# Kernel optimization log

Hardware: AMD Instinct MI355X
Metric: run time of the kernel (lower is better)

## Reference

```python
import jax, jax.numpy as jnp
import numpy as np


def _binarize_ste(w):
    # forward: sign(w) in {-1, +1}; backward: identity (straight-through)
    wb = jnp.where(w >= 0, 1.0, -1.0).astype(w.dtype)
    return w + jax.lax.stop_gradient(wb - w)


def setup_inputs() -> dict:
    key = jax.random.key(0)
    k1, k2 = jax.random.split(key)
    IN, OUT, N = 2048, 2048, 8192
    x = jax.random.normal(k1, (N, IN), dtype=jnp.float32)
    # kaiming_uniform-like init: U(-bound, bound), bound = sqrt(6/in)*? (gain sqrt(5) default in torch)
    bound = float(np.sqrt(6.0 / IN))
    weight = jax.random.uniform(k2, (OUT, IN), dtype=jnp.float32, minval=-bound, maxval=bound)
    bias = jnp.zeros((OUT,), dtype=jnp.float32)
    return {"x": x, "weight": weight, "bias": bias}


def reference(x, weight, bias):
    w_binary = _binarize_ste(weight)  # [out, in], values in {-1, +1}
    # F.linear: x @ W^T + b
    return jnp.einsum('ni,oi->no', x, w_binary) + bias
```

## Files before the change

kernel.cpp:

```cpp
#include <hip/hip_runtime.h>
#include <stdint.h>


typedef __bf16 bf16x8 __attribute__((ext_vector_type(8)));
typedef float f32x16 __attribute__((ext_vector_type(16)));

typedef const __attribute__((address_space(1))) void* gas_ptr;
typedef __attribute__((address_space(3))) void* lds_ptr;

__device__ __forceinline__ unsigned short f2bf_rne(float f) {
    unsigned int u = __builtin_bit_cast(unsigned int, f);
    u += 0x7fffu + ((u >> 16) & 1u);
    return (unsigned short)(u >> 16);
}

__global__ __launch_bounds__(256) void cvt_x_kernel(const float* __restrict__ in,
                                                    unsigned short* __restrict__ out,
                                                    int n8) {
    int i = blockIdx.x * 256 + threadIdx.x;
    if (i >= n8) return;
    const float4* p = reinterpret_cast<const float4*>(in + (size_t)i * 8);
    float4 f0 = p[0], f1 = p[1];
    union { unsigned short s[8]; uint4 v; } o;
    o.s[0] = f2bf_rne(f0.x); o.s[1] = f2bf_rne(f0.y);
    o.s[2] = f2bf_rne(f0.z); o.s[3] = f2bf_rne(f0.w);
    o.s[4] = f2bf_rne(f1.x); o.s[5] = f2bf_rne(f1.y);
    o.s[6] = f2bf_rne(f1.z); o.s[7] = f2bf_rne(f1.w);
    *reinterpret_cast<uint4*>(out + (size_t)i * 8) = o.v;
}

__global__ __launch_bounds__(256) void bin_w_kernel(const float* __restrict__ in,
                                                    unsigned short* __restrict__ out,
                                                    int n4) {
    int i = blockIdx.x * 256 + threadIdx.x;
    if (i >= n4) return;
    float4 f = reinterpret_cast<const float4*>(in)[i];
    union { unsigned short s[4]; uint2 v; } o;
    o.s[0] = (f.x >= 0.f) ? 0x3F80u : 0xBF80u;
    o.s[1] = (f.y >= 0.f) ? 0x3F80u : 0xBF80u;
    o.s[2] = (f.z >= 0.f) ? 0x3F80u : 0xBF80u;
    o.s[3] = (f.w >= 0.f) ? 0x3F80u : 0xBF80u;
    reinterpret_cast<uint2*>(out)[i] = o.v;
}

#define TILE 128
#define BK   64

__global__ __launch_bounds__(256) void gemm_bin_kernel(
    const unsigned short* __restrict__ A,
    const unsigned short* __restrict__ B,
    const float* __restrict__ bias,
    float* __restrict__ C,
    int M, int N, int K)
{
    __shared__ __align__(16) unsigned char smem[32768];
    unsigned short* Als = (unsigned short*)smem;
    unsigned short* Bls = (unsigned short*)(smem + 16384);

    const int tid  = threadIdx.x;
    const int lane = tid & 63;
    const int wave = tid >> 6;
    const int wm   = wave & 1;
    const int wn   = wave >> 1;
    const int bm   = blockIdx.y;
    const int bn   = blockIdx.x;

    const unsigned short* Agb = A + (size_t)(bm * TILE) * K;
    const unsigned short* Bgb = B + (size_t)(bn * TILE) * K;

    f32x16 acc[2][2];
#pragma unroll
    for (int a = 0; a < 2; ++a)
#pragma unroll
        for (int b = 0; b < 2; ++b)
#pragma unroll
            for (int r = 0; r < 16; ++r)
                acc[a][b][r] = 0.f;

    const int lr  = lane & 31;
    const int lk  = lane >> 5;
    const int swz = lane & 7;

    int st_row[4], st_col[4];
#pragma unroll
    for (int j = 0; j < 4; ++j) {
        int g = j * 256 + tid;
        st_row[j] = g >> 3;
        st_col[j] = ((g & 7) ^ (st_row[j] & 7)) * 8;
    }

    for (int k0 = 0; k0 < K; k0 += BK) {
        __syncthreads();

#pragma unroll
        for (int j = 0; j < 4; ++j) {
            int g = j * 256 + tid;
            __builtin_amdgcn_global_load_lds(
                (gas_ptr)(Agb + (size_t)st_row[j] * K + k0 + st_col[j]),
                (lds_ptr)&Als[g * 8], 16, 0, 0);
        }
#pragma unroll
        for (int j = 0; j < 4; ++j) {
            int g = j * 256 + tid;
            __builtin_amdgcn_global_load_lds(
                (gas_ptr)(Bgb + (size_t)st_row[j] * K + k0 + st_col[j]),
                (lds_ptr)&Bls[g * 8], 16, 0, 0);
        }

        __syncthreads();

#pragma unroll
        for (int ks = 0; ks < 4; ++ks) {
            const int c = ks * 2 + lk;
            bf16x8 af[2], bfv[2];
#pragma unroll
            for (int mi = 0; mi < 2; ++mi) {
                int row = wm * 64 + mi * 32 + lr;
                af[mi] = *reinterpret_cast<const bf16x8*>(
                    &Als[(row * 8 + (c ^ swz)) * 8]);
            }
#pragma unroll
            for (int ni = 0; ni < 2; ++ni) {
                int row = wn * 64 + ni * 32 + lr;
                bfv[ni] = *reinterpret_cast<const bf16x8*>(
                    &Bls[(row * 8 + (c ^ swz)) * 8]);
            }
#pragma unroll
            for (int mi = 0; mi < 2; ++mi)
#pragma unroll
                for (int ni = 0; ni < 2; ++ni)
                    acc[mi][ni] = __builtin_amdgcn_mfma_f32_32x32x16_bf16(
                        af[mi], bfv[ni], acc[mi][ni], 0, 0, 0);
        }
    }

    float* eps = (float*)smem + wave * 2048;
    const int c4 = (lane & 15) * 4;
    const int pr = lane >> 4;
    float4 bv = *(const float4*)&bias[bn * TILE + wn * 64 + c4];

#pragma unroll
    for (int mi = 0; mi < 2; ++mi) {
        __syncthreads();
#pragma unroll
        for (int ni = 0; ni < 2; ++ni)
#pragma unroll
            for (int r = 0; r < 16; ++r) {
                int rl = (r & 3) + 8 * (r >> 2) + 4 * lk;
                eps[rl * 64 + ni * 32 + lr] = acc[mi][ni][r];
            }
        __syncthreads();
#pragma unroll
        for (int p = 0; p < 8; ++p) {
            int rl = p * 4 + pr;
            float4 v = *reinterpret_cast<const float4*>(&eps[rl * 64 + c4]);
            float4 o = {v.x + bv.x, v.y + bv.y, v.z + bv.z, v.w + bv.w};
            size_t grow = (size_t)(bm * TILE + wm * 64 + mi * 32 + rl);
            *reinterpret_cast<float4*>(&C[grow * N + bn * TILE + wn * 64 + c4]) = o;
        }
    }
}

extern "C" void kernel_launch(void* const* d_in, const int* in_sizes, int n_in,
                              void* d_out, int out_size, void* d_ws, size_t ws_size,
                              hipStream_t stream) {
    const float* x    = (const float*)d_in[0];
    const float* w    = (const float*)d_in[1];
    const float* bias = (const float*)d_in[2];
    float* out = (float*)d_out;

    const int K = 2048;
    const int N = in_sizes[2];
    const int M = in_sizes[0] / K;

    unsigned short* xb = (unsigned short*)d_ws;
    unsigned short* wb = xb + (size_t)M * K;

    const int nx8 = (M * K) / 8;
    const int nw4 = (N * K) / 4;
    cvt_x_kernel<<<(nx8 + 255) / 256, 256, 0, stream>>>(x, xb, nx8);
    bin_w_kernel<<<(nw4 + 255) / 256, 256, 0, stream>>>(w, wb, nw4);

    dim3 grid(N / TILE, M / TILE);
    gemm_bin_kernel<<<grid, 256, 0, stream>>>(xb, wb, bias, out, M, N, K);
}
```

Before: 200.8 us.

## Double-buffer LDS tiles in bf16 GEMM and fuse input prep kernels

The GEMM main loop now uses two LDS buffers with K-tile 32. The global-to-LDS loads for the next tile are issued before computing on the current one, so memory latency can overlap with MFMA work. The LDS swizzle is adapted to the narrower 4-chunk rows. Separately, the x-to-bf16 conversion and the weight binarization are merged into one launch, with the weight path widened to 8 elements per thread. In exchange there are twice as many barriers per K, and the compiler may insert conservative waits on the async LDS loads that erase much of the overlap.

```diff
diff --git a/kernel.cpp b/kernel.cpp
--- a/kernel.cpp
+++ b/kernel.cpp
@@ -14,37 +14,40 @@
     return (unsigned short)(u >> 16);
 }
 
-__global__ __launch_bounds__(256) void cvt_x_kernel(const float* __restrict__ in,
-                                                    unsigned short* __restrict__ out,
-                                                    int n8) {
+__global__ __launch_bounds__(256) void prep_kernel(
+    const float* __restrict__ x, const float* __restrict__ w,
+    unsigned short* __restrict__ xb, unsigned short* __restrict__ wb,
+    int nx8, int nw8)
+{
     int i = blockIdx.x * 256 + threadIdx.x;
-    if (i >= n8) return;
-    const float4* p = reinterpret_cast<const float4*>(in + (size_t)i * 8);
-    float4 f0 = p[0], f1 = p[1];
-    union { unsigned short s[8]; uint4 v; } o;
-    o.s[0] = f2bf_rne(f0.x); o.s[1] = f2bf_rne(f0.y);
-    o.s[2] = f2bf_rne(f0.z); o.s[3] = f2bf_rne(f0.w);
-    o.s[4] = f2bf_rne(f1.x); o.s[5] = f2bf_rne(f1.y);
-    o.s[6] = f2bf_rne(f1.z); o.s[7] = f2bf_rne(f1.w);
-    *reinterpret_cast<uint4*>(out + (size_t)i * 8) = o.v;
-}
-
-__global__ __launch_bounds__(256) void bin_w_kernel(const float* __restrict__ in,
-                                                    unsigned short* __restrict__ out,
-                                                    int n4) {
-    int i = blockIdx.x * 256 + threadIdx.x;
-    if (i >= n4) return;
-    float4 f = reinterpret_cast<const float4*>(in)[i];
-    union { unsigned short s[4]; uint2 v; } o;
-    o.s[0] = (f.x >= 0.f) ? 0x3F80u : 0xBF80u;
-    o.s[1] = (f.y >= 0.f) ? 0x3F80u : 0xBF80u;
-    o.s[2] = (f.z >= 0.f) ? 0x3F80u : 0xBF80u;
-    o.s[3] = (f.w >= 0.f) ? 0x3F80u : 0xBF80u;
-    reinterpret_cast<uint2*>(out)[i] = o.v;
+    if (i < nx8) {
+        const float4* p = reinterpret_cast<const float4*>(x + (size_t)i * 8);
+        float4 f0 = p[0], f1 = p[1];
+        union { unsigned short s[8]; uint4 v; } o;
+        o.s[0] = f2bf_rne(f0.x); o.s[1] = f2bf_rne(f0.y);
+        o.s[2] = f2bf_rne(f0.z); o.s[3] = f2bf_rne(f0.w);
+        o.s[4] = f2bf_rne(f1.x); o.s[5] = f2bf_rne(f1.y);
+        o.s[6] = f2bf_rne(f1.z); o.s[7] = f2bf_rne(f1.w);
+        *reinterpret_cast<uint4*>(xb + (size_t)i * 8) = o.v;
+    } else if (i < nx8 + nw8) {
+        int j = i - nx8;
+        const float4* p = reinterpret_cast<const float4*>(w + (size_t)j * 8);
+        float4 f0 = p[0], f1 = p[1];
+        union { unsigned short s[8]; uint4 v; } o;
+        o.s[0] = (f0.x >= 0.f) ? 0x3F80u : 0xBF80u;
+        o.s[1] = (f0.y >= 0.f) ? 0x3F80u : 0xBF80u;
+        o.s[2] = (f0.z >= 0.f) ? 0x3F80u : 0xBF80u;
+        o.s[3] = (f0.w >= 0.f) ? 0x3F80u : 0xBF80u;
+        o.s[4] = (f1.x >= 0.f) ? 0x3F80u : 0xBF80u;
+        o.s[5] = (f1.y >= 0.f) ? 0x3F80u : 0xBF80u;
+        o.s[6] = (f1.z >= 0.f) ? 0x3F80u : 0xBF80u;
+        o.s[7] = (f1.w >= 0.f) ? 0x3F80u : 0xBF80u;
+        *reinterpret_cast<uint4*>(wb + (size_t)j * 8) = o.v;
+    }
 }
 
 #define TILE 128
-#define BK   64
+#define BK   32
 
 __global__ __launch_bounds__(256) void gemm_bin_kernel(
     const unsigned short* __restrict__ A,
@@ -54,8 +57,6 @@
     int M, int N, int K)
 {
     __shared__ __align__(16) unsigned char smem[32768];
-    unsigned short* Als = (unsigned short*)smem;
-    unsigned short* Bls = (unsigned short*)(smem + 16384);
 
     const int tid  = threadIdx.x;
     const int lane = tid & 63;
@@ -77,53 +78,54 @@
             for (int r = 0; r < 16; ++r)
                 acc[a][b][r] = 0.f;
 
-    const int lr  = lane & 31;
-    const int lk  = lane >> 5;
-    const int swz = lane & 7;
+    const int lr = lane & 31;
+    const int lk = lane >> 5;
 
-    int st_row[4], st_col[4];
+    int st_row[2], st_col[2];
 #pragma unroll
-    for (int j = 0; j < 4; ++j) {
+    for (int j = 0; j < 2; ++j) {
         int g = j * 256 + tid;
-        st_row[j] = g >> 3;
-        st_col[j] = ((g & 7) ^ (st_row[j] & 7)) * 8;
+        st_row[j] = g >> 2;
+        st_col[j] = (((g & 3) ^ (st_row[j] & 3)) * 8);
     }
 
-    for (int k0 = 0; k0 < K; k0 += BK) {
-        __syncthreads();
-
+    auto stage = [&](int buf, int k0) {
+        unsigned short* Als = (unsigned short*)(smem + buf * 16384);
+        unsigned short* Bls = (unsigned short*)(smem + buf * 16384 + 8192);
 #pragma unroll
-        for (int j = 0; j < 4; ++j) {
+        for (int j = 0; j < 2; ++j) {
             int g = j * 256 + tid;
             __builtin_amdgcn_global_load_lds(
                 (gas_ptr)(Agb + (size_t)st_row[j] * K + k0 + st_col[j]),
                 (lds_ptr)&Als[g * 8], 16, 0, 0);
         }
 #pragma unroll
-        for (int j = 0; j < 4; ++j) {
+        for (int j = 0; j < 2; ++j) {
             int g = j * 256 + tid;
             __builtin_amdgcn_global_load_lds(
                 (gas_ptr)(Bgb + (size_t)st_row[j] * K + k0 + st_col[j]),
                 (lds_ptr)&Bls[g * 8], 16, 0, 0);
         }
+    };
 
-        __syncthreads();
-
+    auto compute = [&](int buf) {
+        const unsigned short* Als = (const unsigned short*)(smem + buf * 16384);
+        const unsigned short* Bls = (const unsigned short*)(smem + buf * 16384 + 8192);
 #pragma unroll
-        for (int ks = 0; ks < 4; ++ks) {
+        for (int ks = 0; ks < 2; ++ks) {
             const int c = ks * 2 + lk;
             bf16x8 af[2], bfv[2];
 #pragma unroll
             for (int mi = 0; mi < 2; ++mi) {
                 int row = wm * 64 + mi * 32 + lr;
                 af[mi] = *reinterpret_cast<const bf16x8*>(
-                    &Als[(row * 8 + (c ^ swz)) * 8]);
+                    &Als[(row * 4 + (c ^ (lr & 3))) * 8]);
             }
 #pragma unroll
             for (int ni = 0; ni < 2; ++ni) {
                 int row = wn * 64 + ni * 32 + lr;
                 bfv[ni] = *reinterpret_cast<const bf16x8*>(
-                    &Bls[(row * 8 + (c ^ swz)) * 8]);
+                    &Bls[(row * 4 + (c ^ (lr & 3))) * 8]);
             }
 #pragma unroll
             for (int mi = 0; mi < 2; ++mi)
@@ -132,6 +134,17 @@
                     acc[mi][ni] = __builtin_amdgcn_mfma_f32_32x32x16_bf16(
                         af[mi], bfv[ni], acc[mi][ni], 0, 0, 0);
         }
+    };
+
+    stage(0, 0);
+    const int kIter = K / BK;
+    for (int it = 0; it < kIter; it += 2) {
+        __syncthreads();
+        stage(1, (it + 1) * BK);
+        compute(0);
+        __syncthreads();
+        if (it + 2 < kIter) stage(0, (it + 2) * BK);
+        compute(1);
     }
 
     float* eps = (float*)smem + wave * 2048;
@@ -177,9 +190,8 @@
     unsigned short* wb = xb + (size_t)M * K;
 
     const int nx8 = (M * K) / 8;
-    const int nw4 = (N * K) / 4;
-    cvt_x_kernel<<<(nx8 + 255) / 256, 256, 0, stream>>>(x, xb, nx8);
-    bin_w_kernel<<<(nw4 + 255) / 256, 256, 0, stream>>>(w, wb, nw4);
+    const int nw8 = (N * K) / 8;
+    prep_kernel<<<(nx8 + nw8 + 255) / 256, 256, 0, stream>>>(x, w, xb, wb, nx8, nw8);
 
     dim3 grid(N / TILE, M / TILE);
     gemm_bin_kernel<<<grid, 256, 0, stream>>>(xb, wb, bias, out, M, N, K);
```

Result: slower. 206.9 us (+3.0%).
